# Optimization experiments

Measured on AMD Instinct MI355X. Metric: run time of the kernel, lower is better.

Reference implementation:

```python
import jax, jax.numpy as jnp
import numpy as np

N_NODES = 50000
N_EDGES = 300000
HID = 256
IN_S, IN_D, IN_E, OUT = 10, 12, 3, 3
K = 2


def _mlp(x, W1, b1, W2, b2):
    # 2-layer MLP: Linear -> relu -> Linear (mlp_layers=2, activation='relu')
    h = jax.nn.relu(x @ W1 + b1)
    return h @ W2 + b2


def setup_inputs() -> dict:
    key = jax.random.key(0)
    ks = jax.random.split(key, 16)

    def w(k, shape):
        return (jax.random.normal(k, shape, jnp.float32) * 0.05)

    z = lambda n: jnp.zeros((n,), jnp.float32)
    return {
        "static_features": jax.random.normal(ks[0], (N_NODES, IN_S), jnp.float32),
        "dynamic_features": jax.random.normal(ks[1], (N_NODES, IN_D), jnp.float32),
        "edge_index": jax.random.randint(ks[2], (2, N_EDGES), 0, N_NODES),
        "edge_attr": jax.random.normal(ks[3], (N_EDGES, IN_E), jnp.float32),
        # static node encoder
        "sW1": w(ks[4], (IN_S, HID)), "sb1": z(HID), "sW2": w(ks[5], (HID, HID)), "sb2": z(HID),
        # dynamic node encoder
        "dW1": w(ks[6], (IN_D, HID)), "db1": z(HID), "dW2": w(ks[7], (HID, HID)), "db2": z(HID),
        # edge encoder (edge_mlp=True)
        "eW1": w(ks[8], (IN_E, HID)), "eb1": z(HID), "eW2": w(ks[9], (HID, HID)), "eb2": z(HID),
        # SWEGNN edge-weight MLP: input [e_ij, x_s_i, x_s_j] -> HID
        "gW1": w(ks[10], (3 * HID, HID)), "gb1": z(HID), "gW2": w(ks[11], (HID, HID)), "gb2": z(HID),
        # decoder
        "oW1": w(ks[12], (HID, HID)), "ob1": z(HID), "oW2": w(ks[13], (HID, OUT)), "ob2": z(OUT),
    }


def reference(static_features, dynamic_features, edge_index, edge_attr,
              sW1, sb1, sW2, sb2, dW1, db1, dW2, db2,
              eW1, eb1, eW2, eb2, gW1, gb1, gW2, gb2,
              oW1, ob1, oW2, ob2):
    # Encoders
    x_s = _mlp(static_features, sW1, sb1, sW2, sb2)   # [N, HID]
    x_d = _mlp(dynamic_features, dW1, db1, dW2, db2)  # [N, HID]
    e = _mlp(edge_attr, eW1, eb1, eW2, eb2)           # [E, HID]

    src, dst = edge_index[0], edge_index[1]

    # Edge-conditioned weights from edge feats + static embeddings of endpoints
    g_in = jnp.concatenate([e, x_s[src], x_s[dst]], axis=-1)  # [E, 3*HID]
    g = _mlp(g_in, gW1, gb1, gW2, gb2)                        # [E, HID]

    # Degree normalization (normalize=True)
    deg = jax.ops.segment_sum(jnp.ones((src.shape[0],), jnp.float32), dst,
                              num_segments=N_NODES)
    inv_deg = (1.0 / jnp.maximum(deg, 1.0))[:, None]  # [N, 1]

    # K hops of SWE message passing: m_ij = g_ij * (h_j - h_i)  (with_gradient=True)
    h = x_d
    for _ in range(K):
        m = g * (h[src] - h[dst])                                  # [E, HID]
        aggr = jax.ops.segment_sum(m, dst, num_segments=N_NODES)   # [N, HID]
        h = h + aggr * inv_deg                                     # residual update

    x = jnp.tanh(h)  # gnn_activation='tanh'
    return _mlp(x, oW1, ob1, oW2, ob2)  # [N, OUT]
```

## Files before the change

kernel.cpp:

```cpp
#include <hip/hip_runtime.h>
#include <hip/hip_bf16.h>

#define N_NODES 50000
#define N_EDGES 300000
#define HID 256
#define AS 264
#define A0S 40

typedef unsigned int uint;
typedef unsigned short ushort;
typedef short bf16x8 __attribute__((ext_vector_type(8)));
typedef unsigned short u16x8 __attribute__((ext_vector_type(8)));
typedef float f32x4 __attribute__((ext_vector_type(4)));

__device__ __forceinline__ float bf2f(ushort u){ union{uint i; float f;} v; v.i=((uint)u)<<16; return v.f; }
__device__ __forceinline__ ushort f2bf(float f){ __hip_bfloat16 h=__float2bfloat16(f); return *reinterpret_cast<ushort*>(&h); }

__device__ __forceinline__ f32x4 mfma16(bf16x8 a, bf16x8 b, f32x4 c){
    return __builtin_amdgcn_mfma_f32_16x16x32_bf16(a, b, c, 0, 0, 0);
}

__device__ __forceinline__ void wave_gemm(const ushort* act, const ushort* __restrict__ WT,
                                          int n0, int lane, f32x4 acc[4][4])
{
    #pragma unroll
    for (int mi=0;mi<4;mi++)
        #pragma unroll
        for (int ni=0;ni<4;ni++) acc[mi][ni]=(f32x4){0.f,0.f,0.f,0.f};
    const int rA=lane&15, kg=(lane>>4)*8;
    __builtin_amdgcn_s_setprio(1);
    #pragma unroll
    for (int kk=0;kk<8;kk++){
        const int ka=kk*32+kg;
        bf16x8 a[4], b[4];
        #pragma unroll
        for (int mi=0;mi<4;mi++) a[mi]=*(const bf16x8*)&act[(mi*16+rA)*AS+ka];
        #pragma unroll
        for (int ni=0;ni<4;ni++) b[ni]=*(const bf16x8*)&WT[(size_t)((n0+ni*16+rA)*HID+ka)];
        #pragma unroll
        for (int mi=0;mi<4;mi++)
            #pragma unroll
            for (int ni=0;ni<4;ni++)
                acc[mi][ni]=mfma16(a[mi], b[ni], acc[mi][ni]);
    }
    __builtin_amdgcn_s_setprio(0);
}

__device__ __forceinline__ void wave_gemm32(const ushort* A0, const ushort* __restrict__ WT32,
                                            int n0, int lane, f32x4 acc[4][4])
{
    const int rA=lane&15, kg=(lane>>4)*8;
    bf16x8 a[4], b[4];
    #pragma unroll
    for (int mi=0;mi<4;mi++) a[mi]=*(const bf16x8*)&A0[(mi*16+rA)*A0S+kg];
    #pragma unroll
    for (int ni=0;ni<4;ni++) b[ni]=*(const bf16x8*)&WT32[(size_t)(n0+ni*16+rA)*32+kg];
    __builtin_amdgcn_s_setprio(1);
    #pragma unroll
    for (int mi=0;mi<4;mi++)
        #pragma unroll
        for (int ni=0;ni<4;ni++)
            acc[mi][ni]=mfma16(a[mi], b[ni], (f32x4){0.f,0.f,0.f,0.f}), void(0);
    __builtin_amdgcn_s_setprio(0);
}

__device__ __forceinline__ void store_c_to_act(ushort* act, const f32x4 acc[4][4],
                                               int colb, int hi, bool relu)
{
    #pragma unroll
    for (int mi=0;mi<4;mi++)
        #pragma unroll
        for (int ni=0;ni<4;ni++)
            #pragma unroll
            for (int r=0;r<4;r++){
                float v=acc[mi][ni][r];
                if (relu) v=fmaxf(v,0.f);
                act[(mi*16+hi*4+r)*AS + colb+ni*16]=f2bf(v);
            }
}

__global__ void combine_weights(const float* __restrict__ sW2, const float* __restrict__ sb2,
                                const float* __restrict__ eW2, const float* __restrict__ eb2,
                                const float* __restrict__ gW1, const float* __restrict__ gb1,
                                const float* __restrict__ dW2, const float* __restrict__ gW2,
                                const float* __restrict__ oW1,
                                const float* __restrict__ eW1, const float* __restrict__ eb1,
                                const float* __restrict__ sW1, const float* __restrict__ sb1,
                                const float* __restrict__ dW1, const float* __restrict__ db1,
                                ushort* __restrict__ WT_A, ushort* __restrict__ WT_B, ushort* __restrict__ WT_E,
                                ushort* __restrict__ WT_d, ushort* __restrict__ WT_g, ushort* __restrict__ WT_o,
                                ushort* __restrict__ WT_e1, ushort* __restrict__ WT_s1, ushort* __restrict__ WT_d1,
                                float* __restrict__ bias_A, float* __restrict__ bias_B)
{
    const int j = threadIdx.x;
    const int i = blockIdx.x;
    const int m = blockIdx.y;
    if (m==6){ if (i<32) WT_e1[j*32+i] = f2bf(i<3 ? eW1[i*HID+j] : (i==3 ? eb1[j] : 0.f)); return; }
    if (m==7){ if (i<32) WT_s1[j*32+i] = f2bf(i<10? sW1[i*HID+j] : (i==10? sb1[j] : 0.f)); return; }
    if (m==8){ if (i<32) WT_d1[j*32+i] = f2bf(i<12? dW1[i*HID+j] : (i==12? db1[j] : 0.f)); return; }
    if (m>=3){
        if (i<HID){
            const float* S = (m==3)? dW2 : (m==4)? gW2 : oW1;
            ushort* D      = (m==3)? WT_d : (m==4)? WT_g : WT_o;
            D[j*HID+i]=f2bf(S[i*HID+j]);
        }
        return;
    }
    const float* L  = (m==2)? eW2 : sW2;
    const float* R  = gW1 + (m==0 ? HID*HID : (m==1 ? 2*HID*HID : 0));
    if (i < HID){
        float acc=0.f;
        for (int k=0;k<HID;k++) acc += L[i*HID+k]*R[k*HID+j];
        (m==0?WT_A:(m==1?WT_B:WT_E))[j*HID+i] = f2bf(acc);
    } else if (m==0){
        float acc=gb1[j];
        for (int k=0;k<HID;k++) acc += sb2[k]*gW1[(HID+k)*HID+j];
        for (int k=0;k<HID;k++) acc += eb2[k]*gW1[k*HID+j];
        bias_A[j]=acc;
    } else if (m==1){
        float acc=0.f;
        for (int k=0;k<HID;k++) acc += sb2[k]*gW1[(2*HID+k)*HID+j];
        bias_B[j]=acc;
    }
}

__global__ __launch_bounds__(256) void node_encode_mfma(
    const float* __restrict__ sfeat, const float* __restrict__ dfeat,
    const ushort* __restrict__ WT_s1, const ushort* __restrict__ WT_d1,
    const ushort* __restrict__ WT_d, const float* __restrict__ db2,
    const ushort* __restrict__ WT_A, const float* __restrict__ bias_A,
    const ushort* __restrict__ WT_B, const float* __restrict__ bias_B,
    ushort* __restrict__ gA, ushort* __restrict__ gB, ushort* __restrict__ h0)
{
    __shared__ ushort act[64*AS];
    __shared__ ushort A0[64*A0S];
    const int tid=threadIdx.x;
    const int n0blk=blockIdx.x*64;
    const int wv=tid>>6, lane=tid&63, n0=wv*64;
    const int rA=lane&15, kg=(lane>>4)*8, hi=lane>>4;
    const int colb=n0+rA;

    {
        const int n=tid>>2, k0=(tid&3)*8;
        const int gn=n0blk+n;
        u16x8 v;
        #pragma unroll
        for (int j=0;j<8;j++){
            const int k=k0+j;
            float f = (gn<N_NODES && k<10)? sfeat[(size_t)gn*10+k] : (k==10? 1.f : 0.f);
            v[j]=f2bf(f);
        }
        *(u16x8*)&A0[n*A0S+k0]=v;
    }
    __syncthreads();
    f32x4 acc[4][4];
    {
        bf16x8 a[4], b[4];
        #pragma unroll
        for (int mi=0;mi<4;mi++) a[mi]=*(const bf16x8*)&A0[(mi*16+rA)*A0S+kg];
        #pragma unroll
        for (int ni=0;ni<4;ni++) b[ni]=*(const bf16x8*)&WT_s1[(size_t)(n0+ni*16+rA)*32+kg];
        #pragma unroll
        for (int mi=0;mi<4;mi++)
            #pragma unroll
            for (int ni=0;ni<4;ni++)
                acc[mi][ni]=mfma16(a[mi], b[ni], (f32x4){0.f,0.f,0.f,0.f});
        store_c_to_act(act, acc, colb, hi, true);
    }
    __syncthreads();
    {
        const int n=tid>>2, k0=(tid&3)*8;
        const int gn=n0blk+n;
        u16x8 v;
        #pragma unroll
        for (int j=0;j<8;j++){
            const int k=k0+j;
            float f = (gn<N_NODES && k<12)? dfeat[(size_t)gn*12+k] : (k==12? 1.f : 0.f);
            v[j]=f2bf(f);
        }
        *(u16x8*)&A0[n*A0S+k0]=v;
    }
    {
        wave_gemm(act, WT_A, n0, lane, acc);
        #pragma unroll
        for (int mi=0;mi<4;mi++){
            #pragma unroll
            for (int ni=0;ni<4;ni++){
                const int col=colb+ni*16; const float bA=bias_A[col];
                #pragma unroll
                for (int r=0;r<4;r++){
                    int rr=mi*16+hi*4+r; int gn=n0blk+rr;
                    if (gn<N_NODES) gA[(size_t)gn*HID+col]=f2bf(acc[mi][ni][r]+bA);
                }
            }
        }
    }
    {
        wave_gemm(act, WT_B, n0, lane, acc);
        #pragma unroll
        for (int mi=0;mi<4;mi++){
            #pragma unroll
            for (int ni=0;ni<4;ni++){
                const int col=colb+ni*16; const float bB=bias_B[col];
                #pragma unroll
                for (int r=0;r<4;r++){
                    int rr=mi*16+hi*4+r; int gn=n0blk+rr;
                    if (gn<N_NODES) gB[(size_t)gn*HID+col]=f2bf(acc[mi][ni][r]+bB);
                }
            }
        }
    }
    __syncthreads();
    {
        bf16x8 a[4], b[4];
        #pragma unroll
        for (int mi=0;mi<4;mi++) a[mi]=*(const bf16x8*)&A0[(mi*16+rA)*A0S+kg];
        #pragma unroll
        for (int ni=0;ni<4;ni++) b[ni]=*(const bf16x8*)&WT_d1[(size_t)(n0+ni*16+rA)*32+kg];
        #pragma unroll
        for (int mi=0;mi<4;mi++)
            #pragma unroll
            for (int ni=0;ni<4;ni++)
                acc[mi][ni]=mfma16(a[mi], b[ni], (f32x4){0.f,0.f,0.f,0.f});
        store_c_to_act(act, acc, colb, hi, true);
    }
    __syncthreads();
    {
        wave_gemm(act, WT_d, n0, lane, acc);
        #pragma unroll
        for (int mi=0;mi<4;mi++){
            #pragma unroll
            for (int ni=0;ni<4;ni++){
                const int col=colb+ni*16; const float bo=db2[col];
                #pragma unroll
                for (int r=0;r<4;r++){
                    int rr=mi*16+hi*4+r; int gn=n0blk+rr;
                    if (gn<N_NODES) h0[(size_t)gn*HID+col]=f2bf(acc[mi][ni][r]+bo);
                }
            }
        }
    }
}

__global__ __launch_bounds__(256) void edge_encode_mfma(
    const float* __restrict__ eattr, const int* __restrict__ eidx,
    const int* __restrict__ csr_src, const int* __restrict__ csr_eid,
    const ushort* __restrict__ WT_e1,
    const ushort* __restrict__ WT_E,
    const ushort* __restrict__ WT_g2, const float* __restrict__ gb2,
    const ushort* __restrict__ gA, const ushort* __restrict__ gB,
    ushort* __restrict__ g_out)
{
    __shared__ ushort act[64*AS];
    __shared__ ushort A0[64*A0S];
    __shared__ int si[64], di[64], ei[64];
    const int tid=threadIdx.x;
    const int bid=blockIdx.x;
    const int s0=((bid&7)*586 + (bid>>3))*64;
    const int wv=tid>>6, lane=tid&63, n0=wv*64;
    const int rA=lane&15, kg=(lane>>4)*8, hi=lane>>4;
    const int colb=n0+rA;

    if (tid<64){
        int s=s0+tid; bool v=s<N_EDGES;
        int eid=v? csr_eid[s]:0;
        si[tid]=v? csr_src[s]:0;
        di[tid]=v? eidx[N_EDGES+eid]:0;
        ei[tid]=eid;
    }
    __syncthreads();
    u16x8 gpa[8];
    {
        const ushort* garow=&gA[(size_t)si[lane]*HID + n0];
        #pragma unroll
        for (int j=0;j<8;j++)
            gpa[j]=*(const u16x8*)&garow[((j+lane)&7)*8];
    }
    {
        const int n=tid>>2, k0=(tid&3)*8;
        const int eid=ei[n];
        u16x8 v;
        #pragma unroll
        for (int j=0;j<8;j++){
            const int k=k0+j;
            float f = (k<3)? eattr[(size_t)eid*3+k] : (k==3? 1.f : 0.f);
            v[j]=f2bf(f);
        }
        *(u16x8*)&A0[n*A0S+k0]=v;
    }
    __syncthreads();
    f32x4 acc[4][4];
    {
        bf16x8 a[4], b[4];
        #pragma unroll
        for (int mi=0;mi<4;mi++) a[mi]=*(const bf16x8*)&A0[(mi*16+rA)*A0S+kg];
        #pragma unroll
        for (int ni=0;ni<4;ni++) b[ni]=*(const bf16x8*)&WT_e1[(size_t)(n0+ni*16+rA)*32+kg];
        #pragma unroll
        for (int mi=0;mi<4;mi++)
            #pragma unroll
            for (int ni=0;ni<4;ni++)
                acc[mi][ni]=mfma16(a[mi], b[ni], (f32x4){0.f,0.f,0.f,0.f});
        store_c_to_act(act, acc, colb, hi, true);
    }
    __syncthreads();
    wave_gemm(act, WT_E, n0, lane, acc);
    __syncthreads();
    store_c_to_act(act, acc, colb, hi, false);
    {
        const ushort* gbrow=&gB[(size_t)di[lane]*HID + n0];
        ushort* arow=&act[lane*AS + n0];
        #pragma unroll
        for (int j=0;j<8;j++){
            const int jb=((j+lane)&7)*8;
            u16x8 av=*(u16x8*)&arow[jb];
            u16x8 gb=*(const u16x8*)&gbrow[jb];
            u16x8 o;
            #pragma unroll
            for (int q=0;q<8;q++)
                o[q]=f2bf(fmaxf(bf2f(av[q])+bf2f(gpa[j][q])+bf2f(gb[q]),0.f));
            *(u16x8*)&arow[jb]=o;
        }
    }
    __syncthreads();
    wave_gemm(act, WT_g2, n0, lane, acc);
    {
        #pragma unroll
        for (int mi=0;mi<4;mi++){
            #pragma unroll
            for (int ni=0;ni<4;ni++){
                const int col=colb+ni*16; const float bg=gb2[col];
                #pragma unroll
                for (int r=0;r<4;r++){
                    const int rr=mi*16+hi*4+r;
                    if (s0+rr<N_EDGES)
                        g_out[(size_t)(s0+rr)*HID+col]=f2bf(acc[mi][ni][r]+bg);
                }
            }
        }
    }
}

__global__ void deg_count(const int* __restrict__ eidx, uint* __restrict__ deg){
    int e=blockIdx.x*blockDim.x+threadIdx.x;
    if (e<N_EDGES) atomicAdd(&deg[eidx[N_EDGES+e]],1u);
}

__global__ void scan_kernel(const uint* __restrict__ deg, uint* __restrict__ row_start){
    __shared__ uint wtot[16];
    __shared__ uint woff[17];
    __shared__ uint carry_s;
    const int tid=threadIdx.x, lane=tid&63, wid=tid>>6;
    if (tid==0) carry_s=0;
    __syncthreads();
    for (uint base=0; base<N_NODES; base+=1024){
        uint idx=base+tid;
        uint v=(idx<N_NODES)? deg[idx]:0u;
        uint s=v;
        #pragma unroll
        for (int d=1; d<64; d<<=1){
            uint t=__shfl_up(s,d,64);
            if (lane>=d) s+=t;
        }
        if (lane==63) wtot[wid]=s;
        __syncthreads();
        if (tid==0){ uint r=0; for (int i=0;i<16;i++){ woff[i]=r; r+=wtot[i]; } woff[16]=r; }
        __syncthreads();
        uint excl = carry_s + woff[wid] + s - v;
        if (idx<N_NODES) row_start[idx]=excl;
        __syncthreads();
        if (tid==0) carry_s += woff[16];
        __syncthreads();
    }
}

__global__ void csr_fill(const int* __restrict__ eidx, const uint* __restrict__ row_start,
                         uint* __restrict__ cursor, int* __restrict__ csr_src, int* __restrict__ csr_eid){
    int e=blockIdx.x*blockDim.x+threadIdx.x;
    if (e>=N_EDGES) return;
    int d=eidx[N_EDGES+e];
    uint pos=atomicAdd(&cursor[d],1u);
    uint s=row_start[d]+pos;
    csr_src[s]=eidx[e];
    csr_eid[s]=e;
}

__global__ __launch_bounds__(256) void hop_kernel(
    const ushort* __restrict__ h_in, ushort* __restrict__ h_out,
    const ushort* __restrict__ g, const int* __restrict__ csr_src,
    const uint* __restrict__ row_start, const uint* __restrict__ deg)
{
    const int gw=(blockIdx.x*blockDim.x+threadIdx.x)>>6;
    if (gw>=N_NODES) return;
    const int c0=(threadIdx.x&63)*4;
    ushort4 hd4=*(const ushort4*)&h_in[(size_t)gw*HID+c0];
    float4 hd; hd.x=bf2f(hd4.x); hd.y=bf2f(hd4.y); hd.z=bf2f(hd4.z); hd.w=bf2f(hd4.w);
    float4 acc=make_float4(0,0,0,0);
    const uint st=row_start[gw], len=deg[gw];
    for (uint u=0;u<len;u++){
        uint s=st+u;
        int sn=csr_src[s];
        ushort4 g4=*(const ushort4*)&g[(size_t)s*HID+c0];
        ushort4 hs4=*(const ushort4*)&h_in[(size_t)sn*HID+c0];
        acc.x += bf2f(g4.x)*(bf2f(hs4.x)-hd.x);
        acc.y += bf2f(g4.y)*(bf2f(hs4.y)-hd.y);
        acc.z += bf2f(g4.z)*(bf2f(hs4.z)-hd.z);
        acc.w += bf2f(g4.w)*(bf2f(hs4.w)-hd.w);
    }
    const float inv=1.f/fmaxf((float)len,1.f);
    ushort4 o; o.x=f2bf(hd.x+acc.x*inv); o.y=f2bf(hd.y+acc.y*inv);
               o.z=f2bf(hd.z+acc.z*inv); o.w=f2bf(hd.w+acc.w*inv);
    *(ushort4*)&h_out[(size_t)gw*HID+c0]=o;
}

__global__ __launch_bounds__(256) void decoder_mfma(
    const ushort* __restrict__ h, const ushort* __restrict__ WT_o,
    const float* __restrict__ ob1, const float* __restrict__ oW2, const float* __restrict__ ob2,
    float* __restrict__ out)
{
    __shared__ ushort act[64*AS];
    const int tid=threadIdx.x, n0blk=blockIdx.x*64;
    const int wv=tid>>6, lane=tid&63, n0=wv*64, colb=n0+(lane&15);
    {
        const int row=tid>>2, cc=(tid&3)*64;
        const int gn=n0blk+row;
        #pragma unroll
        for (int k=0;k<64;k+=8){
            u16x8 t;
            if (gn<N_NODES){
                u16x8 v=*(const u16x8*)&h[(size_t)gn*HID+cc+k];
                #pragma unroll
                for (int j=0;j<8;j++) t[j]=f2bf(tanhf(bf2f(v[j])));
            } else {
                #pragma unroll
                for (int j=0;j<8;j++) t[j]=0;
            }
            *(u16x8*)&act[row*AS+cc+k]=t;
        }
    }
    __syncthreads();
    f32x4 acc[4][4];
    wave_gemm(act, WT_o, n0, lane, acc);
    __syncthreads();
    #pragma unroll
    for (int mi=0;mi<4;mi++){
        #pragma unroll
        for (int ni=0;ni<4;ni++){
            const int col=colb+ni*16; const float b1=ob1[col];
            #pragma unroll
            for (int r=0;r<4;r++){
                const int rr=mi*16+(lane>>4)*4+r;
                act[rr*AS+col]=f2bf(fmaxf(acc[mi][ni][r]+b1,0.f));
            }
        }
    }
    __syncthreads();
    if (tid<192){
        const int n=tid/3, o=tid-n*3;
        float a=ob2[o];
        for (int k=0;k<HID;k++) a+=bf2f(act[n*AS+k])*oW2[k*3+o];
        const int gn=n0blk+n;
        if (gn<N_NODES) out[(size_t)gn*3+o]=a;
    }
}

extern "C" void kernel_launch(void* const* d_in, const int* in_sizes, int n_in,
                              void* d_out, int out_size, void* d_ws, size_t ws_size,
                              hipStream_t stream)
{
    (void)in_sizes; (void)n_in; (void)out_size;
    const float* sfeat=(const float*)d_in[0];
    const float* dfeat=(const float*)d_in[1];
    const int*   eidx =(const int*)  d_in[2];
    const float* eattr=(const float*)d_in[3];
    const float* sW1=(const float*)d_in[4];  const float* sb1=(const float*)d_in[5];
    const float* sW2=(const float*)d_in[6];  const float* sb2=(const float*)d_in[7];
    const float* dW1=(const float*)d_in[8];  const float* db1=(const float*)d_in[9];
    const float* dW2=(const float*)d_in[10]; const float* db2=(const float*)d_in[11];
    const float* eW1=(const float*)d_in[12]; const float* eb1=(const float*)d_in[13];
    const float* eW2=(const float*)d_in[14]; const float* eb2=(const float*)d_in[15];
    const float* gW1=(const float*)d_in[16]; const float* gb1=(const float*)d_in[17];
    const float* gW2=(const float*)d_in[18]; const float* gb2=(const float*)d_in[19];
    const float* oW1=(const float*)d_in[20]; const float* ob1=(const float*)d_in[21];
    const float* oW2=(const float*)d_in[22]; const float* ob2=(const float*)d_in[23];
    float* out=(float*)d_out;

    char* p=(char*)d_ws;
    size_t used=0;
    auto alloc=[&](size_t bytes)->char*{
        char* r=p+used; used += (bytes+255)&~(size_t)255; return r;
    };
    ushort* WT_A=(ushort*)alloc(HID*HID*2);
    ushort* WT_B=(ushort*)alloc(HID*HID*2);
    ushort* WT_E=(ushort*)alloc(HID*HID*2);
    ushort* WT_d=(ushort*)alloc(HID*HID*2);
    ushort* WT_g=(ushort*)alloc(HID*HID*2);
    ushort* WT_o=(ushort*)alloc(HID*HID*2);
    ushort* WT_e1=(ushort*)alloc(HID*32*2);
    ushort* WT_s1=(ushort*)alloc(HID*32*2);
    ushort* WT_d1=(ushort*)alloc(HID*32*2);
    float* bias_A=(float*)alloc(HID*4);
    float* bias_B=(float*)alloc(HID*4);
    ushort* gA=(ushort*)alloc((size_t)N_NODES*HID*2);
    ushort* gB=(ushort*)alloc((size_t)N_NODES*HID*2);
    ushort* g =(ushort*)alloc((size_t)N_EDGES*HID*2);
    ushort* h0=(ushort*)alloc((size_t)N_NODES*HID*2);
    uint* deg      =(uint*)alloc(N_NODES*4);
    uint* row_start=(uint*)alloc(N_NODES*4);
    uint* cursor   =(uint*)alloc(N_NODES*4);
    int* csr_src=(int*)alloc(N_EDGES*4);
    int* csr_eid=(int*)alloc(N_EDGES*4);
    ushort* h1=gA;

    if (used > ws_size) return;

    hipMemsetAsync(deg, 0, N_NODES*4, stream);
    hipMemsetAsync(cursor, 0, N_NODES*4, stream);

    combine_weights<<<dim3(HID+1,9),256,0,stream>>>(sW2,sb2,eW2,eb2,gW1,gb1,dW2,gW2,oW1,eW1,eb1,sW1,sb1,dW1,db1,
                                                    WT_A,WT_B,WT_E,WT_d,WT_g,WT_o,WT_e1,WT_s1,WT_d1,bias_A,bias_B);
    node_encode_mfma<<<(N_NODES+63)/64,256,0,stream>>>(sfeat,dfeat,WT_s1,WT_d1,WT_d,db2,WT_A,bias_A,WT_B,bias_B,gA,gB,h0);
    deg_count<<<(N_EDGES+255)/256,256,0,stream>>>(eidx,deg);
    scan_kernel<<<1,1024,0,stream>>>(deg,row_start);
    csr_fill<<<(N_EDGES+255)/256,256,0,stream>>>(eidx,row_start,cursor,csr_src,csr_eid);
    edge_encode_mfma<<<(N_EDGES+63)/64,256,0,stream>>>(eattr,eidx,csr_src,csr_eid,WT_e1,WT_E,WT_g,gb2,gA,gB,g);
    hop_kernel<<<N_NODES/4,256,0,stream>>>(h0,h1,g,csr_src,row_start,deg);
    hop_kernel<<<N_NODES/4,256,0,stream>>>(h1,h0,g,csr_src,row_start,deg);
    decoder_mfma<<<(N_NODES+63)/64,256,0,stream>>>(h0,WT_o,ob1,oW2,ob2,out);
}
```

Baseline: 591.9 us.

## Double edge-encoder tile to 128 edges per 512-thread block

The edge encoder block now processes 128 edges with 8 waves arranged 2x4 over rows and columns, instead of 64 edges with 4 waves. Each B-weight fragment read from global memory is therefore reused across more rows per block. The gA prefetch is moved next to the gB gather, and the s_setprio calls plus an unused helper are removed. In exchange the block uses roughly twice the LDS, which may lower the number of resident blocks per CU.

Result: no change. 581.0 us (-1.8%).

```diff
diff --git a/kernel.cpp b/kernel.cpp
--- a/kernel.cpp
+++ b/kernel.cpp
@@ -28,7 +28,6 @@
         #pragma unroll
         for (int ni=0;ni<4;ni++) acc[mi][ni]=(f32x4){0.f,0.f,0.f,0.f};
     const int rA=lane&15, kg=(lane>>4)*8;
-    __builtin_amdgcn_s_setprio(1);
     #pragma unroll
     for (int kk=0;kk<8;kk++){
         const int ka=kk*32+kg;
@@ -43,25 +42,6 @@
             for (int ni=0;ni<4;ni++)
                 acc[mi][ni]=mfma16(a[mi], b[ni], acc[mi][ni]);
     }
-    __builtin_amdgcn_s_setprio(0);
-}
-
-__device__ __forceinline__ void wave_gemm32(const ushort* A0, const ushort* __restrict__ WT32,
-                                            int n0, int lane, f32x4 acc[4][4])
-{
-    const int rA=lane&15, kg=(lane>>4)*8;
-    bf16x8 a[4], b[4];
-    #pragma unroll
-    for (int mi=0;mi<4;mi++) a[mi]=*(const bf16x8*)&A0[(mi*16+rA)*A0S+kg];
-    #pragma unroll
-    for (int ni=0;ni<4;ni++) b[ni]=*(const bf16x8*)&WT32[(size_t)(n0+ni*16+rA)*32+kg];
-    __builtin_amdgcn_s_setprio(1);
-    #pragma unroll
-    for (int mi=0;mi<4;mi++)
-        #pragma unroll
-        for (int ni=0;ni<4;ni++)
-            acc[mi][ni]=mfma16(a[mi], b[ni], (f32x4){0.f,0.f,0.f,0.f}), void(0);
-    __builtin_amdgcn_s_setprio(0);
 }
 
 __device__ __forceinline__ void store_c_to_act(ushort* act, const f32x4 acc[4][4],
@@ -242,7 +222,7 @@
     }
 }
 
-__global__ __launch_bounds__(256) void edge_encode_mfma(
+__global__ __launch_bounds__(512) void edge_encode_mfma(
     const float* __restrict__ eattr, const int* __restrict__ eidx,
     const int* __restrict__ csr_src, const int* __restrict__ csr_eid,
     const ushort* __restrict__ WT_e1,
@@ -251,17 +231,19 @@
     const ushort* __restrict__ gA, const ushort* __restrict__ gB,
     ushort* __restrict__ g_out)
 {
-    __shared__ ushort act[64*AS];
-    __shared__ ushort A0[64*A0S];
-    __shared__ int si[64], di[64], ei[64];
+    __shared__ ushort act[128*AS];
+    __shared__ ushort A0[128*A0S];
+    __shared__ int si[128], di[128], ei[128];
     const int tid=threadIdx.x;
     const int bid=blockIdx.x;
-    const int s0=((bid&7)*586 + (bid>>3))*64;
-    const int wv=tid>>6, lane=tid&63, n0=wv*64;
+    const int s0=((bid&7)*293 + (bid>>3))*128;
+    const int wv=tid>>6, lane=tid&63;
+    const int wm=wv>>2, wn=wv&3;
+    const int m0=wm*64, n0=wn*64;
     const int rA=lane&15, kg=(lane>>4)*8, hi=lane>>4;
     const int colb=n0+rA;
 
-    if (tid<64){
+    if (tid<128){
         int s=s0+tid; bool v=s<N_EDGES;
         int eid=v? csr_eid[s]:0;
         si[tid]=v? csr_src[s]:0;
@@ -269,13 +251,6 @@
         ei[tid]=eid;
     }
     __syncthreads();
-    u16x8 gpa[8];
-    {
-        const ushort* garow=&gA[(size_t)si[lane]*HID + n0];
-        #pragma unroll
-        for (int j=0;j<8;j++)
-            gpa[j]=*(const u16x8*)&garow[((j+lane)&7)*8];
-    }
     {
         const int n=tid>>2, k0=(tid&3)*8;
         const int eid=ei[n];
@@ -293,7 +268,7 @@
     {
         bf16x8 a[4], b[4];
         #pragma unroll
-        for (int mi=0;mi<4;mi++) a[mi]=*(const bf16x8*)&A0[(mi*16+rA)*A0S+kg];
+        for (int mi=0;mi<4;mi++) a[mi]=*(const bf16x8*)&A0[(m0+mi*16+rA)*A0S+kg];
         #pragma unroll
         for (int ni=0;ni<4;ni++) b[ni]=*(const bf16x8*)&WT_e1[(size_t)(n0+ni*16+rA)*32+kg];
         #pragma unroll
@@ -301,29 +276,32 @@
             #pragma unroll
             for (int ni=0;ni<4;ni++)
                 acc[mi][ni]=mfma16(a[mi], b[ni], (f32x4){0.f,0.f,0.f,0.f});
-        store_c_to_act(act, acc, colb, hi, true);
-    }
-    __syncthreads();
-    wave_gemm(act, WT_E, n0, lane, acc);
-    __syncthreads();
-    store_c_to_act(act, acc, colb, hi, false);
-    {
-        const ushort* gbrow=&gB[(size_t)di[lane]*HID + n0];
-        ushort* arow=&act[lane*AS + n0];
+        store_c_to_act(act + m0*AS, acc, colb, hi, true);
+    }
+    __syncthreads();
+    wave_gemm(act + m0*AS, WT_E, n0, lane, acc);
+    __syncthreads();
+    store_c_to_act(act + m0*AS, acc, colb, hi, false);
+    {
+        const int row=m0+lane;
+        const ushort* garow=&gA[(size_t)si[row]*HID + n0];
+        const ushort* gbrow=&gB[(size_t)di[row]*HID + n0];
+        ushort* arow=&act[row*AS + n0];
         #pragma unroll
         for (int j=0;j<8;j++){
             const int jb=((j+lane)&7)*8;
             u16x8 av=*(u16x8*)&arow[jb];
+            u16x8 ga=*(const u16x8*)&garow[jb];
             u16x8 gb=*(const u16x8*)&gbrow[jb];
             u16x8 o;
             #pragma unroll
             for (int q=0;q<8;q++)
-                o[q]=f2bf(fmaxf(bf2f(av[q])+bf2f(gpa[j][q])+bf2f(gb[q]),0.f));
+                o[q]=f2bf(fmaxf(bf2f(av[q])+bf2f(ga[q])+bf2f(gb[q]),0.f));
             *(u16x8*)&arow[jb]=o;
         }
     }
     __syncthreads();
-    wave_gemm(act, WT_g2, n0, lane, acc);
+    wave_gemm(act + m0*AS, WT_g2, n0, lane, acc);
     {
         #pragma unroll
         for (int mi=0;mi<4;mi++){
@@ -332,7 +310,7 @@
                 const int col=colb+ni*16; const float bg=gb2[col];
                 #pragma unroll
                 for (int r=0;r<4;r++){
-                    const int rr=mi*16+hi*4+r;
+                    const int rr=m0+mi*16+hi*4+r;
                     if (s0+rr<N_EDGES)
                         g_out[(size_t)(s0+rr)*HID+col]=f2bf(acc[mi][ni][r]+bg);
                 }
@@ -523,7 +501,7 @@
     deg_count<<<(N_EDGES+255)/256,256,0,stream>>>(eidx,deg);
     scan_kernel<<<1,1024,0,stream>>>(deg,row_start);
     csr_fill<<<(N_EDGES+255)/256,256,0,stream>>>(eidx,row_start,cursor,csr_src,csr_eid);
-    edge_encode_mfma<<<(N_EDGES+63)/64,256,0,stream>>>(eattr,eidx,csr_src,csr_eid,WT_e1,WT_E,WT_g,gb2,gA,gB,g);
+    edge_encode_mfma<<<(N_EDGES+127)/128,512,0,stream>>>(eattr,eidx,csr_src,csr_eid,WT_e1,WT_E,WT_g,gb2,gA,gB,g);
     hop_kernel<<<N_NODES/4,256,0,stream>>>(h0,h1,g,csr_src,row_start,deg);
     hop_kernel<<<N_NODES/4,256,0,stream>>>(h1,h0,g,csr_src,row_start,deg);
     decoder_mfma<<<(N_NODES+63)/64,256,0,stream>>>(h0,WT_o,ob1,oW2,ob2,out);
```

## Split fused edge encoder into two GEMM kernels with intermediate buffer

Applied to the files above, without the earlier changes.

Splits the single edge encoder kernel into edge_gemm1, which computes the edge MLP and writes it to the g buffer, and edge_gemm2, which gathers the gA/gB node projections, adds them, applies relu and runs the second GEMM in place. It also stores the destination per CSR slot so the second kernel avoids an indirect edge_index lookup, and it drops the s_setprio hints. The apparent aim is to cut register and latency pressure from holding gathered rows across the first GEMMs, at the cost of writing and re-reading an extra E×256 bf16 intermediate.

Result: slower. 629.2 us (+6.3%).

```diff
diff --git a/kernel.cpp b/kernel.cpp
--- a/kernel.cpp
+++ b/kernel.cpp
@@ -28,7 +28,6 @@
         #pragma unroll
         for (int ni=0;ni<4;ni++) acc[mi][ni]=(f32x4){0.f,0.f,0.f,0.f};
     const int rA=lane&15, kg=(lane>>4)*8;
-    __builtin_amdgcn_s_setprio(1);
     #pragma unroll
     for (int kk=0;kk<8;kk++){
         const int ka=kk*32+kg;
@@ -43,25 +42,6 @@
             for (int ni=0;ni<4;ni++)
                 acc[mi][ni]=mfma16(a[mi], b[ni], acc[mi][ni]);
     }
-    __builtin_amdgcn_s_setprio(0);
-}
-
-__device__ __forceinline__ void wave_gemm32(const ushort* A0, const ushort* __restrict__ WT32,
-                                            int n0, int lane, f32x4 acc[4][4])
-{
-    const int rA=lane&15, kg=(lane>>4)*8;
-    bf16x8 a[4], b[4];
-    #pragma unroll
-    for (int mi=0;mi<4;mi++) a[mi]=*(const bf16x8*)&A0[(mi*16+rA)*A0S+kg];
-    #pragma unroll
-    for (int ni=0;ni<4;ni++) b[ni]=*(const bf16x8*)&WT32[(size_t)(n0+ni*16+rA)*32+kg];
-    __builtin_amdgcn_s_setprio(1);
-    #pragma unroll
-    for (int mi=0;mi<4;mi++)
-        #pragma unroll
-        for (int ni=0;ni<4;ni++)
-            acc[mi][ni]=mfma16(a[mi], b[ni], (f32x4){0.f,0.f,0.f,0.f}), void(0);
-    __builtin_amdgcn_s_setprio(0);
 }
 
 __device__ __forceinline__ void store_c_to_act(ushort* act, const f32x4 acc[4][4],
@@ -242,18 +222,14 @@
     }
 }
 
-__global__ __launch_bounds__(256) void edge_encode_mfma(
-    const float* __restrict__ eattr, const int* __restrict__ eidx,
-    const int* __restrict__ csr_src, const int* __restrict__ csr_eid,
-    const ushort* __restrict__ WT_e1,
-    const ushort* __restrict__ WT_E,
-    const ushort* __restrict__ WT_g2, const float* __restrict__ gb2,
-    const ushort* __restrict__ gA, const ushort* __restrict__ gB,
-    ushort* __restrict__ g_out)
+__global__ __launch_bounds__(256) void edge_gemm1(
+    const float* __restrict__ eattr, const int* __restrict__ csr_eid,
+    const ushort* __restrict__ WT_e1, const ushort* __restrict__ WT_E,
+    ushort* __restrict__ X)
 {
     __shared__ ushort act[64*AS];
     __shared__ ushort A0[64*A0S];
-    __shared__ int si[64], di[64], ei[64];
+    __shared__ int ei[64];
     const int tid=threadIdx.x;
     const int bid=blockIdx.x;
     const int s0=((bid&7)*586 + (bid>>3))*64;
@@ -261,21 +237,8 @@
     const int rA=lane&15, kg=(lane>>4)*8, hi=lane>>4;
     const int colb=n0+rA;
 
-    if (tid<64){
-        int s=s0+tid; bool v=s<N_EDGES;
-        int eid=v? csr_eid[s]:0;
-        si[tid]=v? csr_src[s]:0;
-        di[tid]=v? eidx[N_EDGES+eid]:0;
-        ei[tid]=eid;
-    }
-    __syncthreads();
-    u16x8 gpa[8];
-    {
-        const ushort* garow=&gA[(size_t)si[lane]*HID + n0];
-        #pragma unroll
-        for (int j=0;j<8;j++)
-            gpa[j]=*(const u16x8*)&garow[((j+lane)&7)*8];
-    }
+    if (tid<64){ int s=s0+tid; ei[tid]=(s<N_EDGES)? csr_eid[s]:0; }
+    __syncthreads();
     {
         const int n=tid>>2, k0=(tid&3)*8;
         const int eid=ei[n];
@@ -307,22 +270,55 @@
     wave_gemm(act, WT_E, n0, lane, acc);
     __syncthreads();
     store_c_to_act(act, acc, colb, hi, false);
-    {
-        const ushort* gbrow=&gB[(size_t)di[lane]*HID + n0];
-        ushort* arow=&act[lane*AS + n0];
+    __syncthreads();
+    for (int i=tid;i<64*32;i+=256){
+        const int row=i>>5, ch=i&31;
+        const int s=s0+row;
+        if (s<N_EDGES)
+            *(u16x8*)&X[(size_t)s*HID + ch*8] = *(const u16x8*)&act[row*AS + ch*8];
+    }
+}
+
+__global__ __launch_bounds__(256) void edge_gemm2(
+    const int* __restrict__ csr_src, const int* __restrict__ csr_dst,
+    const ushort* __restrict__ gA, const ushort* __restrict__ gB,
+    const ushort* __restrict__ WT_g2, const float* __restrict__ gb2,
+    ushort* __restrict__ X)
+{
+    __shared__ ushort act[64*AS];
+    const int tid=threadIdx.x;
+    const int bid=blockIdx.x;
+    const int s0=((bid&7)*586 + (bid>>3))*64;
+    const int wv=tid>>6, lane=tid&63, n0=wv*64;
+    const int rA=lane&15, hi=lane>>4;
+    const int colb=n0+rA;
+
+    {
+        const int row=tid>>2, cs=(tid&3)*64;
+        const int s=s0+row;
+        const int sc=(s<N_EDGES)? s : N_EDGES-1;
+        const int si=csr_src[sc], di=csr_dst[sc];
+        const ushort* xr=&X [(size_t)sc*HID+cs];
+        const ushort* ga=&gA[(size_t)si*HID+cs];
+        const ushort* gb=&gB[(size_t)di*HID+cs];
+        u16x8 xv[8], av[8], bv[8];
+        #pragma unroll
+        for (int j=0;j<8;j++) xv[j]=*(const u16x8*)&xr[j*8];
+        #pragma unroll
+        for (int j=0;j<8;j++) av[j]=*(const u16x8*)&ga[j*8];
+        #pragma unroll
+        for (int j=0;j<8;j++) bv[j]=*(const u16x8*)&gb[j*8];
         #pragma unroll
         for (int j=0;j<8;j++){
-            const int jb=((j+lane)&7)*8;
-            u16x8 av=*(u16x8*)&arow[jb];
-            u16x8 gb=*(const u16x8*)&gbrow[jb];
             u16x8 o;
             #pragma unroll
             for (int q=0;q<8;q++)
-                o[q]=f2bf(fmaxf(bf2f(av[q])+bf2f(gpa[j][q])+bf2f(gb[q]),0.f));
-            *(u16x8*)&arow[jb]=o;
-        }
-    }
-    __syncthreads();
+                o[q]=f2bf(fmaxf(bf2f(xv[j][q])+bf2f(av[j][q])+bf2f(bv[j][q]),0.f));
+            *(u16x8*)&act[row*AS+cs+j*8]=o;
+        }
+    }
+    __syncthreads();
+    f32x4 acc[4][4];
     wave_gemm(act, WT_g2, n0, lane, acc);
     {
         #pragma unroll
@@ -334,7 +330,7 @@
                 for (int r=0;r<4;r++){
                     const int rr=mi*16+hi*4+r;
                     if (s0+rr<N_EDGES)
-                        g_out[(size_t)(s0+rr)*HID+col]=f2bf(acc[mi][ni][r]+bg);
+                        X[(size_t)(s0+rr)*HID+col]=f2bf(acc[mi][ni][r]+bg);
                 }
             }
         }
@@ -375,13 +371,15 @@
 }
 
 __global__ void csr_fill(const int* __restrict__ eidx, const uint* __restrict__ row_start,
-                         uint* __restrict__ cursor, int* __restrict__ csr_src, int* __restrict__ csr_eid){
+                         uint* __restrict__ cursor, int* __restrict__ csr_src,
+                         int* __restrict__ csr_dst, int* __restrict__ csr_eid){
     int e=blockIdx.x*blockDim.x+threadIdx.x;
     if (e>=N_EDGES) return;
     int d=eidx[N_EDGES+e];
     uint pos=atomicAdd(&cursor[d],1u);
     uint s=row_start[d]+pos;
     csr_src[s]=eidx[e];
+    csr_dst[s]=d;
     csr_eid[s]=e;
 }
 
@@ -509,6 +507,7 @@
     uint* row_start=(uint*)alloc(N_NODES*4);
     uint* cursor   =(uint*)alloc(N_NODES*4);
     int* csr_src=(int*)alloc(N_EDGES*4);
+    int* csr_dst=(int*)alloc(N_EDGES*4);
     int* csr_eid=(int*)alloc(N_EDGES*4);
     ushort* h1=gA;
 
@@ -522,8 +521,9 @@
     node_encode_mfma<<<(N_NODES+63)/64,256,0,stream>>>(sfeat,dfeat,WT_s1,WT_d1,WT_d,db2,WT_A,bias_A,WT_B,bias_B,gA,gB,h0);
     deg_count<<<(N_EDGES+255)/256,256,0,stream>>>(eidx,deg);
     scan_kernel<<<1,1024,0,stream>>>(deg,row_start);
-    csr_fill<<<(N_EDGES+255)/256,256,0,stream>>>(eidx,row_start,cursor,csr_src,csr_eid);
-    edge_encode_mfma<<<(N_EDGES+63)/64,256,0,stream>>>(eattr,eidx,csr_src,csr_eid,WT_e1,WT_E,WT_g,gb2,gA,gB,g);
+    csr_fill<<<(N_EDGES+255)/256,256,0,stream>>>(eidx,row_start,cursor,csr_src,csr_dst,csr_eid);
+    edge_gemm1<<<(N_EDGES+63)/64,256,0,stream>>>(eattr,csr_eid,WT_e1,WT_E,g);
+    edge_gemm2<<<(N_EDGES+63)/64,256,0,stream>>>(csr_src,csr_dst,gA,gB,WT_g,gb2,g);
     hop_kernel<<<N_NODES/4,256,0,stream>>>(h0,h1,g,csr_src,row_start,deg);
     hop_kernel<<<N_NODES/4,256,0,stream>>>(h1,h0,g,csr_src,row_start,deg);
     decoder_mfma<<<(N_NODES+63)/64,256,0,stream>>>(h0,WT_o,ob1,oW2,ob2,out);
```
